# Kernel tuning notes

Hardware: AMD Instinct MI355X
Metric: run time of the kernel (lower is better)

The kernel has to match this reference:

```python
import jax, jax.numpy as jnp
import numpy as np

B, SIZE, TRACK = 4096, 1024, 1024  # batch, input size, tracker_size


def setup_inputs() -> dict:
    key = jax.random.key(0)
    ks = jax.random.split(key, 9)
    s = 0.02  # small init scale to keep gates in a sane range
    return {
        "top_buf_h": jax.random.normal(ks[0], (B, SIZE), jnp.float32),
        "top_stack1_h": jax.random.normal(ks[1], (B, SIZE), jnp.float32),
        "top_stack2_h": jax.random.normal(ks[2], (B, SIZE), jnp.float32),
        "h_prev": jax.random.normal(ks[3], (B, TRACK), jnp.float32),
        "c_prev": jax.random.normal(ks[4], (B, TRACK), jnp.float32),
        "W_buf": jax.random.normal(ks[5], (SIZE, 4 * TRACK), jnp.float32) * s,
        "W_stack1": jax.random.normal(ks[6], (SIZE, 4 * TRACK), jnp.float32) * s,
        "W_stack2": jax.random.normal(ks[7], (SIZE, 4 * TRACK), jnp.float32) * s,
        "W_lateral": jax.random.normal(ks[8], (TRACK, 4 * TRACK), jnp.float32) * s,
        "b_lateral": jnp.zeros((4 * TRACK,), jnp.float32),
    }


def reference(top_buf_h, top_stack1_h, top_stack2_h, h_prev, c_prev,
              W_buf, W_stack1, W_stack2, W_lateral, b_lateral):
    # Fused tracker step: 3 bias-free projections + lateral projection (with bias)
    gates = (top_buf_h @ W_buf
             + top_stack1_h @ W_stack1
             + top_stack2_h @ W_stack2
             + h_prev @ W_lateral
             + b_lateral)                      # [B, 4*TRACK]
    # SPINN lstm(c_prev, gates): chunk order (a, i, f, o)
    a, i, f, o = jnp.split(gates, 4, axis=1)
    c = jnp.tanh(a) * jax.nn.sigmoid(i) + jax.nn.sigmoid(f) * c_prev
    h = jax.nn.sigmoid(o) * jnp.tanh(c)
    return (h, c)
```

## Files before the change

kernel.cpp:

```cpp
#include <hip/hip_runtime.h>


typedef __bf16 bf16x8 __attribute__((ext_vector_type(8)));
typedef float  f32x4  __attribute__((ext_vector_type(4)));

__device__ __forceinline__ unsigned short f2bf(float x) {
    unsigned int u = __builtin_bit_cast(unsigned int, x);
    u = (u + 0x7fffu + ((u >> 16) & 1u)) >> 16;
    return (unsigned short)u;
}

__device__ __forceinline__ void gl2lds16(const unsigned short* g, unsigned short* l) {
    __builtin_amdgcn_global_load_lds(
        (const __attribute__((address_space(1))) unsigned int*)g,
        (__attribute__((address_space(3))) unsigned int*)l,
        16, 0, 0);
}

__device__ __forceinline__ float sigf(float x) {
    return __builtin_amdgcn_rcpf(1.f + __expf(-x));
}
__device__ __forceinline__ float tanh_fast(float x) {
    return 2.f * __builtin_amdgcn_rcpf(1.f + __expf(-2.f * x)) - 1.f;
}


__global__ void convert_AB(const float* __restrict__ A0, const float* __restrict__ A1,
                           const float* __restrict__ A2, const float* __restrict__ A3,
                           const float* __restrict__ Wb, const float* __restrict__ W1,
                           const float* __restrict__ W2, const float* __restrict__ Wl,
                           unsigned short* __restrict__ Abf,
                           unsigned short* __restrict__ Bt) {
    __shared__ float t[32][33];
    if (blockIdx.x < 16384) {
        int idx = blockIdx.x * 256 + threadIdx.x;
        int e0  = idx * 4;
        int b   = e0 >> 12;
        int k   = e0 & 4095;
        const float* S = (k < 1024) ? A0 : (k < 2048) ? A1 : (k < 3072) ? A2 : A3;
        int col = k & 1023;
        const float4 v = *reinterpret_cast<const float4*>(S + (size_t)b * 1024 + col);
        ushort4 o;
        o.x = f2bf(v.x); o.y = f2bf(v.y); o.z = f2bf(v.z); o.w = f2bf(v.w);
        *reinterpret_cast<ushort4*>(Abf + (size_t)b * 4096 + k) = o;
    } else {
        int tile = blockIdx.x - 16384;
        int jt = tile & 127, kt = tile >> 7;
        int j0 = jt * 32, k0 = kt * 32;
        int ksel = k0 >> 10;
        const float* S = (ksel == 0) ? Wb : (ksel == 1) ? W1 : (ksel == 2) ? W2 : Wl;
        int kloc = k0 & 1023;
        int tx = threadIdx.x & 31, ty = threadIdx.x >> 5;
#pragma unroll
        for (int i = 0; i < 4; ++i) {
            int r = ty + i * 8;
            t[r][tx] = S[(size_t)(kloc + r) * 4096 + j0 + tx];
        }
        __syncthreads();
        int g = j0 >> 10;
        int nbase = j0 & 1023;
#pragma unroll
        for (int i = 0; i < 4; ++i) {
            int jj = ty + i * 8;
            int u  = nbase + jj;
            int p  = (u >> 6) * 256 + ((u >> 4) & 3) * 64 + g * 16 + (u & 15);
            Bt[(size_t)p * 4096 + k0 + tx] = f2bf(t[tx][jj]);
        }
    }
}


__global__ __launch_bounds__(512, 2) void gemm_lstm(
        const unsigned short* __restrict__ A,
        const unsigned short* __restrict__ Bt,
        const float* __restrict__ bias,
        const float* __restrict__ cprev,
        float* __restrict__ out) {
    __shared__ unsigned short lds[65536];
#define ASB(b) (lds + (b) * 16384)
#define BSB(b) (lds + 32768 + (b) * 16384)

    const int tid  = threadIdx.x;
    const int wid  = tid >> 6;
    const int lane = tid & 63;
    const int wm = wid >> 2, wn = wid & 3;
    const int lr = lane & 15, lq = lane >> 4;
    const int bm = blockIdx.y, bc = blockIdx.x;

    const int X0 = wid * 1024 + lane * 16;
    const int rs = X0 >> 7;
    const int cs = ((X0 & 127) ^ ((rs & 7) << 4)) >> 1;
    const unsigned short* Agb = A  + ((size_t)(bm * 256 + rs)) * 4096 + cs;
    const unsigned short* Bgb = Bt + ((size_t)(bc * 256 + rs)) * 4096 + cs;

    const int swz = (lr & 7) << 4;
    const int ca0 = ((lq * 16) ^ swz) >> 1;
    const int ca1 = ((64 + lq * 16) ^ swz) >> 1;

    f32x4 acc[8][4] = {};

#define STAGE_A(b, h, kt) do {                                               \
        unsigned short* _d = ASB(b) + (h) * 8192 + wid * 512;                \
        const unsigned short* _s = Agb + (size_t)((h) * 128) * 4096 + (kt) * 64; \
        gl2lds16(_s, _d);                                                    \
        gl2lds16(_s + 64 * 4096, _d + 4096);                                 \
    } while (0)
#define STAGE_B(b, h, kt) do {                                               \
        unsigned short* _d = BSB(b) + (h) * 8192 + wid * 512;                \
        const unsigned short* _s = Bgb + (size_t)((h) * 128) * 4096 + (kt) * 64; \
        gl2lds16(_s, _d);                                                    \
        gl2lds16(_s + 64 * 4096, _d + 4096);                                 \
    } while (0)
#define LDA(buf, mi, cax) (*reinterpret_cast<const bf16x8*>((buf) + (wm * 128 + (mi) * 16 + lr) * 64 + (cax)))
#define LDB(buf, ni, cax) (*reinterpret_cast<const bf16x8*>((buf) + (wn * 64  + (ni) * 16 + lr) * 64 + (cax)))
#define RD_A(DST, BUF, MI0) do {                                             \
        _Pragma("unroll")                                                    \
        for (int m = 0; m < 2; ++m) {                                        \
            DST[m][0] = LDA(BUF, (MI0) + m, ca0);                            \
            DST[m][1] = LDA(BUF, (MI0) + m, ca1);                            \
        } } while (0)
#define RD_B(DST, BUF) do {                                                  \
        _Pragma("unroll")                                                    \
        for (int n = 0; n < 4; ++n) {                                        \
            DST[n][0] = LDB(BUF, n, ca0);                                    \
            DST[n][1] = LDB(BUF, n, ca1);                                    \
        } } while (0)
#define SBAR() __builtin_amdgcn_s_barrier()
#define SFENCE() __builtin_amdgcn_sched_barrier(0)
#define VMFENCE() asm volatile("s_waitcnt vmcnt(4)" ::: "memory")
#define MFMA16(P, AF, BF)                                                    \
        __builtin_amdgcn_s_setprio(1);                                       \
        _Pragma("unroll")                                                    \
        for (int m = 0; m < 2; ++m)                                          \
        _Pragma("unroll")                                                    \
        for (int ks = 0; ks < 2; ++ks)                                       \
        _Pragma("unroll")                                                    \
        for (int ni = 0; ni < 4; ++ni)                                       \
            acc[(P)*2 + m][ni] = __builtin_amdgcn_mfma_f32_16x16x32_bf16(    \
                AF[m][ks], BF[ni][ks], acc[(P)*2 + m][ni], 0, 0, 0);         \
        __builtin_amdgcn_s_setprio(0)

#define KITER(T, PAR) do {                                                   \
        const unsigned short* Ac = ASB(PAR);                                 \
        const unsigned short* Bc = BSB(PAR);                                 \
        const int ktA = ((T) < 63) ? (T) + 1 : 63;                           \
        const int ktB = ((T) < 62) ? (T) + 2 : 63;                           \
        STAGE_A(PAR ^ 1, 0, ktA);                                            \
        STAGE_A(PAR ^ 1, 1, ktA);                                            \
        bf16x8 bfr[4][2];                                                    \
        bf16x8 af[2][2];                                                     \
        RD_B(bfr, Bc);                                                       \
        RD_A(af, Ac, 0);                                                     \
        SFENCE();                                                            \
        MFMA16(0, af, bfr);                                                  \
        SFENCE();                                                            \
        SBAR();     \
        STAGE_B(PAR, 0, ktB);                                                \
        STAGE_B(PAR, 1, ktB);                                                \
        RD_A(af, Ac, 2);                                                     \
        SFENCE();                                                            \
        MFMA16(1, af, bfr);                                                  \
        SFENCE();                                                            \
        RD_A(af, Ac, 4);                                                     \
        SFENCE();                                                            \
        MFMA16(2, af, bfr);                                                  \
        SFENCE();                                                            \
        RD_A(af, Ac, 6);                                                     \
        SFENCE();                                                            \
        MFMA16(3, af, bfr);                                                  \
        VMFENCE();                                                           \
        SBAR();                          \
    } while (0)

    STAGE_A(0, 0, 0); STAGE_A(0, 1, 0);
    STAGE_B(0, 0, 0); STAGE_B(0, 1, 0);
    STAGE_B(1, 0, 1); STAGE_B(1, 1, 1);
    VMFENCE();
    SBAR();

    for (int u = 0; u < 32; ++u) {
        KITER(2 * u, 0);
        KITER(2 * u + 1, 1);
    }

    const int un = bc * 64 + wn * 16 + lr;
    const float ba  = bias[un];
    const float bi  = bias[1024 + un];
    const float bfv = bias[2048 + un];
    const float bo  = bias[3072 + un];
    float* outh = out;
    float* outc = out + (size_t)4096 * 1024;

#pragma unroll
    for (int mi = 0; mi < 8; ++mi) {
        const int r0 = bm * 256 + wm * 128 + mi * 16 + lq * 4;
#pragma unroll
        for (int r = 0; r < 4; ++r) {
            const size_t off = (size_t)(r0 + r) * 1024 + un;
            const float a  = acc[mi][0][r] + ba;
            const float ii = acc[mi][1][r] + bi;
            const float ff = acc[mi][2][r] + bfv;
            const float oo = acc[mi][3][r] + bo;
            const float c  = tanh_fast(a) * sigf(ii) + sigf(ff) * cprev[off];
            outh[off] = sigf(oo) * tanh_fast(c);
            outc[off] = c;
        }
    }
#undef STAGE_A
#undef STAGE_B
#undef LDA
#undef LDB
#undef RD_A
#undef RD_B
#undef SBAR
#undef SFENCE
#undef VMFENCE
#undef MFMA16
#undef KITER
#undef ASB
#undef BSB
}


extern "C" void kernel_launch(void* const* d_in, const int* in_sizes, int n_in,
                              void* d_out, int out_size, void* d_ws, size_t ws_size,
                              hipStream_t stream) {
    const float* top_buf = (const float*)d_in[0];
    const float* s1      = (const float*)d_in[1];
    const float* s2      = (const float*)d_in[2];
    const float* hprev   = (const float*)d_in[3];
    const float* cprev   = (const float*)d_in[4];
    const float* Wb      = (const float*)d_in[5];
    const float* W1      = (const float*)d_in[6];
    const float* W2      = (const float*)d_in[7];
    const float* Wl      = (const float*)d_in[8];
    const float* bl      = (const float*)d_in[9];

    unsigned short* Abf = (unsigned short*)d_ws;
    unsigned short* Bt  = Abf + (size_t)4096 * 4096;

    convert_AB<<<32768, 256, 0, stream>>>(top_buf, s1, s2, hprev,
                                          Wb, W1, W2, Wl, Abf, Bt);

    dim3 grid(16, 16);
    gemm_lstm<<<grid, 512, 0, stream>>>(Abf, Bt, bl, cprev, (float*)d_out);
}
```

Baseline: 147.7 us.

## Shrink GEMM block tile to 256x128 with 4 waves and K-step 32

```diff
diff --git a/kernel.cpp b/kernel.cpp
--- a/kernel.cpp
+++ b/kernel.cpp
@@ -63,127 +63,118 @@
         for (int i = 0; i < 4; ++i) {
             int jj = ty + i * 8;
             int u  = nbase + jj;
-            int p  = (u >> 6) * 256 + ((u >> 4) & 3) * 64 + g * 16 + (u & 15);
+            int p  = (u >> 5) * 128 + ((u >> 4) & 1) * 64 + g * 16 + (u & 15);
             Bt[(size_t)p * 4096 + k0 + tx] = f2bf(t[tx][jj]);
         }
     }
 }
 
 
-__global__ __launch_bounds__(512, 2) void gemm_lstm(
+__global__ __launch_bounds__(256, 2) void gemm_lstm(
         const unsigned short* __restrict__ A,
         const unsigned short* __restrict__ Bt,
         const float* __restrict__ bias,
         const float* __restrict__ cprev,
         float* __restrict__ out) {
-    __shared__ unsigned short lds[65536];
-#define ASB(b) (lds + (b) * 16384)
-#define BSB(b) (lds + 32768 + (b) * 16384)
+    __shared__ unsigned short lds[24576];
+#define ASB(b) (lds + (b) * 8192)
+#define BSB(b) (lds + 16384 + (b) * 4096)
 
     const int tid  = threadIdx.x;
     const int wid  = tid >> 6;
     const int lane = tid & 63;
-    const int wm = wid >> 2, wn = wid & 3;
+    const int wm = wid >> 1, wn = wid & 1;
     const int lr = lane & 15, lq = lane >> 4;
     const int bm = blockIdx.y, bc = blockIdx.x;
 
     const int X0 = wid * 1024 + lane * 16;
-    const int rs = X0 >> 7;
-    const int cs = ((X0 & 127) ^ ((rs & 7) << 4)) >> 1;
+    const int rs = X0 >> 6;
+    const int cs = ((X0 & 63) ^ ((rs & 3) << 4)) >> 1;
     const unsigned short* Agb = A  + ((size_t)(bm * 256 + rs)) * 4096 + cs;
-    const unsigned short* Bgb = Bt + ((size_t)(bc * 256 + rs)) * 4096 + cs;
-
-    const int swz = (lr & 7) << 4;
-    const int ca0 = ((lq * 16) ^ swz) >> 1;
-    const int ca1 = ((64 + lq * 16) ^ swz) >> 1;
+    const unsigned short* Bgb = Bt + ((size_t)(bc * 128 + rs)) * 4096 + cs;
+
+    const int ca = ((lq * 16) ^ ((lr & 3) << 4)) >> 1;
 
     f32x4 acc[8][4] = {};
 
 #define STAGE_A(b, h, kt) do {                                               \
-        unsigned short* _d = ASB(b) + (h) * 8192 + wid * 512;                \
-        const unsigned short* _s = Agb + (size_t)((h) * 128) * 4096 + (kt) * 64; \
+        unsigned short* _d = ASB(b) + (h) * 4096 + wid * 512;                \
+        const unsigned short* _s = Agb + (size_t)((h) * 128) * 4096 + (kt) * 32; \
         gl2lds16(_s, _d);                                                    \
-        gl2lds16(_s + 64 * 4096, _d + 4096);                                 \
-    } while (0)
-#define STAGE_B(b, h, kt) do {                                               \
-        unsigned short* _d = BSB(b) + (h) * 8192 + wid * 512;                \
-        const unsigned short* _s = Bgb + (size_t)((h) * 128) * 4096 + (kt) * 64; \
+        gl2lds16(_s + 64 * 4096, _d + 2048);                                 \
+    } while (0)
+#define STAGE_B(b, kt) do {                                                  \
+        unsigned short* _d = BSB(b) + wid * 512;                             \
+        const unsigned short* _s = Bgb + (size_t)(kt) * 32;                  \
         gl2lds16(_s, _d);                                                    \
-        gl2lds16(_s + 64 * 4096, _d + 4096);                                 \
-    } while (0)
-#define LDA(buf, mi, cax) (*reinterpret_cast<const bf16x8*>((buf) + (wm * 128 + (mi) * 16 + lr) * 64 + (cax)))
-#define LDB(buf, ni, cax) (*reinterpret_cast<const bf16x8*>((buf) + (wn * 64  + (ni) * 16 + lr) * 64 + (cax)))
+        gl2lds16(_s + 64 * 4096, _d + 2048);                                 \
+    } while (0)
+#define LDA(buf, mi) (*reinterpret_cast<const bf16x8*>((buf) + (wm * 128 + (mi) * 16 + lr) * 32 + ca))
+#define LDB(buf, ni) (*reinterpret_cast<const bf16x8*>((buf) + (wn * 64  + (ni) * 16 + lr) * 32 + ca))
 #define RD_A(DST, BUF, MI0) do {                                             \
         _Pragma("unroll")                                                    \
-        for (int m = 0; m < 2; ++m) {                                        \
-            DST[m][0] = LDA(BUF, (MI0) + m, ca0);                            \
-            DST[m][1] = LDA(BUF, (MI0) + m, ca1);                            \
-        } } while (0)
+        for (int m = 0; m < 2; ++m) DST[m] = LDA(BUF, (MI0) + m);            \
+    } while (0)
 #define RD_B(DST, BUF) do {                                                  \
         _Pragma("unroll")                                                    \
-        for (int n = 0; n < 4; ++n) {                                        \
-            DST[n][0] = LDB(BUF, n, ca0);                                    \
-            DST[n][1] = LDB(BUF, n, ca1);                                    \
-        } } while (0)
+        for (int n = 0; n < 4; ++n) DST[n] = LDB(BUF, n);                    \
+    } while (0)
 #define SBAR() __builtin_amdgcn_s_barrier()
 #define SFENCE() __builtin_amdgcn_sched_barrier(0)
-#define VMFENCE() asm volatile("s_waitcnt vmcnt(4)" ::: "memory")
-#define MFMA16(P, AF, BF)                                                    \
+#define VMFENCE() asm volatile("s_waitcnt vmcnt(2)" ::: "memory")
+#define MFMA8(P, AF, BF)                                                     \
         __builtin_amdgcn_s_setprio(1);                                       \
         _Pragma("unroll")                                                    \
         for (int m = 0; m < 2; ++m)                                          \
-        _Pragma("unroll")                                                    \
-        for (int ks = 0; ks < 2; ++ks)                                       \
         _Pragma("unroll")                                                    \
         for (int ni = 0; ni < 4; ++ni)                                       \
             acc[(P)*2 + m][ni] = __builtin_amdgcn_mfma_f32_16x16x32_bf16(    \
-                AF[m][ks], BF[ni][ks], acc[(P)*2 + m][ni], 0, 0, 0);         \
+                AF[m], BF[ni], acc[(P)*2 + m][ni], 0, 0, 0);                 \
         __builtin_amdgcn_s_setprio(0)
 
 #define KITER(T, PAR) do {                                                   \
         const unsigned short* Ac = ASB(PAR);                                 \
         const unsigned short* Bc = BSB(PAR);                                 \
-        const int ktA = ((T) < 63) ? (T) + 1 : 63;                           \
-        const int ktB = ((T) < 62) ? (T) + 2 : 63;                           \
+        const int ktA = ((T) < 127) ? (T) + 1 : 127;                         \
+        const int ktB = ((T) < 126) ? (T) + 2 : 127;                         \
         STAGE_A(PAR ^ 1, 0, ktA);                                            \
         STAGE_A(PAR ^ 1, 1, ktA);                                            \
-        bf16x8 bfr[4][2];                                                    \
-        bf16x8 af[2][2];                                                     \
+        bf16x8 bfr[4];                                                       \
+        bf16x8 af[2];                                                        \
         RD_B(bfr, Bc);                                                       \
         RD_A(af, Ac, 0);                                                     \
         SFENCE();                                                            \
-        MFMA16(0, af, bfr);                                                  \
+        MFMA8(0, af, bfr);                                                   \
         SFENCE();                                                            \
         SBAR();     \
-        STAGE_B(PAR, 0, ktB);                                                \
-        STAGE_B(PAR, 1, ktB);                                                \
+        STAGE_B(PAR, ktB);                                                   \
         RD_A(af, Ac, 2);                                                     \
         SFENCE();                                                            \
-        MFMA16(1, af, bfr);                                                  \
+        MFMA8(1, af, bfr);                                                   \
         SFENCE();                                                            \
         RD_A(af, Ac, 4);                                                     \
         SFENCE();                                                            \
-        MFMA16(2, af, bfr);                                                  \
+        MFMA8(2, af, bfr);                                                   \
         SFENCE();                                                            \
         RD_A(af, Ac, 6);                                                     \
         SFENCE();                                                            \
-        MFMA16(3, af, bfr);                                                  \
+        MFMA8(3, af, bfr);                                                   \
         VMFENCE();                                                           \
         SBAR();                          \
     } while (0)
 
     STAGE_A(0, 0, 0); STAGE_A(0, 1, 0);
-    STAGE_B(0, 0, 0); STAGE_B(0, 1, 0);
-    STAGE_B(1, 0, 1); STAGE_B(1, 1, 1);
+    STAGE_B(0, 0);
+    STAGE_B(1, 1);
     VMFENCE();
     SBAR();
 
-    for (int u = 0; u < 32; ++u) {
+    for (int u = 0; u < 64; ++u) {
         KITER(2 * u, 0);
         KITER(2 * u + 1, 1);
     }
 
-    const int un = bc * 64 + wn * 16 + lr;
+    const int un = bc * 32 + wn * 16 + lr;
     const float ba  = bias[un];
     const float bi  = bias[1024 + un];
     const float bfv = bias[2048 + un];
@@ -215,7 +206,7 @@
 #undef SBAR
 #undef SFENCE
 #undef VMFENCE
-#undef MFMA16
+#undef MFMA8
 #undef KITER
 #undef ASB
 #undef BSB
@@ -242,6 +233,6 @@
     convert_AB<<<32768, 256, 0, stream>>>(top_buf, s1, s2, hprev,
                                           Wb, W1, W2, Wl, Abf, Bt);
 
-    dim3 grid(16, 16);
-    gemm_lstm<<<grid, 512, 0, stream>>>(Abf, Bt, bl, cprev, (float*)d_out);
-}
+    dim3 grid(32, 16);
+    gemm_lstm<<<grid, 256, 0, stream>>>(Abf, Bt, bl, cprev, (float*)d_out);
+}
```

Measured after the change: 170.7 us. 1.16x slower.
